# Optimization experiments

Hardware: AMD Instinct MI355X
Metric: run time of the kernel (lower is better)

Reference implementation:

```python
import jax, jax.numpy as jnp
import numpy as np

SIGMA = 0.2
BN_EPS = 1e-5


def setup_inputs() -> dict:
    key = jax.random.key(0)
    k1, k2, k3, k4 = jax.random.split(key, 4)
    B, F, K, M = 8, 16384, 3, 64
    normals = jax.random.normal(k1, (B, 3, F), dtype=jnp.float32)
    # normalize to unit vectors (face normals), keeps math well-conditioned
    normals = normals / jnp.linalg.norm(normals, axis=1, keepdims=True)
    weight_alpha = jax.random.uniform(k2, (1, M, 4), dtype=jnp.float32) * np.pi
    weight_beta = jax.random.uniform(k3, (1, M, 4), dtype=jnp.float32) * 2 * np.pi
    bn_gamma = jnp.ones((M,), dtype=jnp.float32)
    bn_beta = jnp.zeros((M,), dtype=jnp.float32)
    neighbor_index = jax.random.randint(k4, (B, F, K), 0, F, dtype=jnp.int64)
    return {"normals": normals, "weight_alpha": weight_alpha,
            "weight_beta": weight_beta, "bn_gamma": bn_gamma,
            "bn_beta": bn_beta, "neighbor_index": neighbor_index}


def reference(normals, weight_alpha, weight_beta, bn_gamma, bn_beta, neighbor_index):
    # normals: [B, 3, F]; neighbor_index: [B, F, K]
    B, _, F = normals.shape
    K = neighbor_index.shape[-1]
    # kernel points on unit sphere from spherical angles: [3, M, 4]
    sa, ca = jnp.sin(weight_alpha), jnp.cos(weight_alpha)
    sb, cb = jnp.sin(weight_beta), jnp.cos(weight_beta)
    w = jnp.concatenate([sa * cb, sa * sb, ca], axis=0)  # [3, M, 4]

    nt = jnp.transpose(normals, (0, 2, 1))  # [B, F, 3]
    # gather neighbor normals per batch: [B, F, K, 3]
    neigh = jax.vmap(lambda n, idx: n[idx])(nt, neighbor_index)
    # points per face: center + K neighbors -> [B, F, K+1, 3]
    pts = jnp.concatenate([nt[:, :, None, :], neigh], axis=2)

    # squared distance via expansion: ||p||^2 + ||w||^2 - 2 p.w
    dot = jnp.einsum('bfic,cmj->bmfij', pts, w)        # [B, M, F, K+1, 4]
    p2 = jnp.sum(pts * pts, axis=-1)                   # [B, F, K+1]
    w2 = jnp.sum(w * w, axis=0)                        # [M, 4]
    dist = (p2[:, None, :, :, None] + w2[None, :, None, None, :] - 2.0 * dot)

    feat = jnp.sum(jnp.exp(dist / (-2.0 * SIGMA ** 2)), axis=(3, 4))
    feat = feat / float((K + 1) * 4)                   # [B, M, F]

    # BatchNorm1d (training-mode batch stats over B and F per channel M)
    mean = jnp.mean(feat, axis=(0, 2), keepdims=True)
    var = jnp.var(feat, axis=(0, 2), keepdims=True)
    xhat = (feat - mean) / jnp.sqrt(var + BN_EPS)
    out = xhat * bn_gamma[None, :, None] + bn_beta[None, :, None]
    return jax.nn.relu(out)
```

## Files before the change

kernel.cpp:

```cpp
#include <hip/hip_runtime.h>

#define B_DIM 8
#define F_DIM 16384
#define K_DIM 3
#define M_DIM 64
#define MCH   16
#define LOG2E 1.4426950408889634f

#define WS_Q 16384

__global__ __launch_bounds__(256, 4) void fkc_feat_kernel(
    const float* __restrict__ normals,
    const float* __restrict__ walpha,
    const float* __restrict__ wbeta,
    const int*   __restrict__ nidx,
    float* __restrict__ feat_out,
    float* __restrict__ ws)
{
    __shared__ float4 sW[MCH * 4];
    __shared__ float sRS[MCH][32];
    __shared__ float sRQ[MCH][32];

    const int tid = threadIdx.x;
    const int b  = blockIdx.x >> 7;
    const int mc = (blockIdx.x >> 5) & 3;
    const int fc = blockIdx.x & 31;

    if (tid < MCH * 4) {
        int idx = mc * MCH * 4 + tid;
        float a = walpha[idx], bb = wbeta[idx];
        float sa = sinf(a), ca = cosf(a);
        float sb = sinf(bb), cb = cosf(bb);
        float wx = sa * cb, wy = sa * sb, wz = ca;
        float w2 = wx * wx + wy * wy + wz * wz;
        sW[tid] = make_float4(wx * 25.0f * LOG2E, wy * 25.0f * LOG2E,
                              wz * 25.0f * LOG2E, -12.5f * LOG2E * (w2 + 1.0f));
    }
    __syncthreads();

    const int f0 = (fc << 9) + tid * 2;
    const float* nb = normals + (size_t)b * 3 * F_DIM;

    float pxA[4], pyA[4], pzA[4], pxB[4], pyB[4], pzB[4];
    {
        float2 vx = *(const float2*)(nb + f0);
        float2 vy = *(const float2*)(nb + F_DIM + f0);
        float2 vz = *(const float2*)(nb + 2 * F_DIM + f0);
        pxA[0] = vx.x; pxB[0] = vx.y;
        pyA[0] = vy.x; pyB[0] = vy.y;
        pzA[0] = vz.x; pzB[0] = vz.y;
    }
    {
        const int* ib = nidx + ((size_t)b * F_DIM + f0) * K_DIM;
#pragma unroll
        for (int k = 0; k < K_DIM; ++k) {
            int id = ib[k];
            pxA[k + 1] = nb[id]; pyA[k + 1] = nb[F_DIM + id]; pzA[k + 1] = nb[2 * F_DIM + id];
            id = ib[k + 3];
            pxB[k + 1] = nb[id]; pyB[k + 1] = nb[F_DIM + id]; pzB[k + 1] = nb[2 * F_DIM + id];
        }
    }

    const int wave = tid >> 6, lane = tid & 63;
    float* outb = feat_out + ((size_t)b * M_DIM + mc * MCH) * F_DIM + f0;
#pragma unroll 2
    for (int m = 0; m < MCH; ++m) {
        float a0 = 0.f, a1 = 0.f, a2 = 0.f, a3 = 0.f;
        float b0 = 0.f, b1 = 0.f, b2 = 0.f, b3 = 0.f;
#pragma unroll
        for (int j = 0; j < 4; ++j) {
            float4 w = sW[m * 4 + j];
            a0 += __builtin_amdgcn_exp2f(fmaf(w.x, pxA[0], fmaf(w.y, pyA[0], fmaf(w.z, pzA[0], w.w))));
            a1 += __builtin_amdgcn_exp2f(fmaf(w.x, pxA[1], fmaf(w.y, pyA[1], fmaf(w.z, pzA[1], w.w))));
            a2 += __builtin_amdgcn_exp2f(fmaf(w.x, pxA[2], fmaf(w.y, pyA[2], fmaf(w.z, pzA[2], w.w))));
            a3 += __builtin_amdgcn_exp2f(fmaf(w.x, pxA[3], fmaf(w.y, pyA[3], fmaf(w.z, pzA[3], w.w))));
            b0 += __builtin_amdgcn_exp2f(fmaf(w.x, pxB[0], fmaf(w.y, pyB[0], fmaf(w.z, pzB[0], w.w))));
            b1 += __builtin_amdgcn_exp2f(fmaf(w.x, pxB[1], fmaf(w.y, pyB[1], fmaf(w.z, pzB[1], w.w))));
            b2 += __builtin_amdgcn_exp2f(fmaf(w.x, pxB[2], fmaf(w.y, pyB[2], fmaf(w.z, pzB[2], w.w))));
            b3 += __builtin_amdgcn_exp2f(fmaf(w.x, pxB[3], fmaf(w.y, pyB[3], fmaf(w.z, pzB[3], w.w))));
        }
        float fA = ((a0 + a1) + (a2 + a3)) * (1.0f / 16.0f);
        float fB = ((b0 + b1) + (b2 + b3)) * (1.0f / 16.0f);
        *(float2*)(outb + (size_t)m * F_DIM) = make_float2(fA, fB);

        float s = fA + fB;
        float q = fA * fA + fB * fB;
        s += __shfl_xor(s, 8, 64);  q += __shfl_xor(q, 8, 64);
        s += __shfl_xor(s, 16, 64); q += __shfl_xor(q, 16, 64);
        s += __shfl_xor(s, 32, 64); q += __shfl_xor(q, 32, 64);
        if (lane < 8) { sRS[m][wave * 8 + lane] = s; sRQ[m][wave * 8 + lane] = q; }
    }
    __syncthreads();

    {
        const int m = tid >> 4, j = tid & 15;
        float s = sRS[m][j] + sRS[m][j + 16];
        float q = sRQ[m][j] + sRQ[m][j + 16];
        s += __shfl_xor(s, 1, 64);  q += __shfl_xor(q, 1, 64);
        s += __shfl_xor(s, 2, 64);  q += __shfl_xor(q, 2, 64);
        s += __shfl_xor(s, 4, 64);  q += __shfl_xor(q, 4, 64);
        s += __shfl_xor(s, 8, 64);  q += __shfl_xor(q, 8, 64);
        if (j == 0) {
            int slot = (mc * MCH + m) * 256 + b * 32 + fc;
            ws[slot] = s;
            ws[WS_Q + slot] = q;
        }
    }
}

__global__ __launch_bounds__(256) void fkc_bn_kernel(
    float* __restrict__ out,
    const float* __restrict__ gamma,
    const float* __restrict__ beta,
    const float* __restrict__ ws)
{
    __shared__ float sS[4], sQ[4];
    __shared__ float sAC[2];
    const int row = blockIdx.x;
    const int m = row & 63;
    const int tid = threadIdx.x;
    const int wave = tid >> 6, lane = tid & 63;

    {
        float s = ws[m * 256 + tid];
        float q = ws[WS_Q + m * 256 + tid];
#pragma unroll
        for (int off = 32; off >= 1; off >>= 1) {
            s += __shfl_xor(s, off, 64);
            q += __shfl_xor(q, off, 64);
        }
        if (lane == 0) { sS[wave] = s; sQ[wave] = q; }
    }
    __syncthreads();
    if (tid == 0) {
        float s = (sS[0] + sS[1]) + (sS[2] + sS[3]);
        float q = (sQ[0] + sQ[1]) + (sQ[2] + sQ[3]);
        const float invcnt = 1.0f / (float)(B_DIM * F_DIM);
        float mean = s * invcnt;
        float var  = q * invcnt - mean * mean;
        float inv  = rsqrtf(var + 1e-5f);
        float A = gamma[m] * inv;
        sAC[0] = A;
        sAC[1] = beta[m] - mean * A;
    }
    __syncthreads();

    const float A = sAC[0], C = sAC[1];
    float4* p4 = (float4*)(out + (size_t)row * F_DIM);
#pragma unroll
    for (int i = 0; i < 16; ++i) {
        float4 v = p4[tid + i * 256];
        v.x = fmaxf(fmaf(v.x, A, C), 0.0f);
        v.y = fmaxf(fmaf(v.y, A, C), 0.0f);
        v.z = fmaxf(fmaf(v.z, A, C), 0.0f);
        v.w = fmaxf(fmaf(v.w, A, C), 0.0f);
        p4[tid + i * 256] = v;
    }
}

extern "C" void kernel_launch(void* const* d_in, const int* in_sizes, int n_in,
                              void* d_out, int out_size, void* d_ws, size_t ws_size,
                              hipStream_t stream)
{
    const float* normals = (const float*)d_in[0];
    const float* walpha  = (const float*)d_in[1];
    const float* wbeta   = (const float*)d_in[2];
    const float* gamma   = (const float*)d_in[3];
    const float* beta    = (const float*)d_in[4];
    const int*   nidx    = (const int*)d_in[5];
    float* out = (float*)d_out;
    float* ws  = (float*)d_ws;

    hipLaunchKernelGGL(fkc_feat_kernel, dim3(1024), dim3(256), 0, stream,
                       normals, walpha, wbeta, nidx, out, ws);
    hipLaunchKernelGGL(fkc_bn_kernel, dim3(B_DIM * M_DIM), dim3(256), 0, stream,
                       out, gamma, beta, ws);
}
```

Before: 53.19 us.

## Precompute kernel-point table in separate launch and halve channel chunk per block

Weight trig is moved into a tiny one-block kernel that writes a float4 table to the workspace. The feature kernel reads it through global/scalar loads instead of an LDS staging step with a block barrier. The channel chunk drops from 16 to 8, doubling the grid to 2048 blocks with higher occupancy bounds, and the m loop is fully unrolled. The 1/16 scaling is folded into the BN kernel's affine constants. The cost is an extra kernel launch and a second read of the neighbor gathers per block, since each face's gathers are now repeated across 8 channel chunks instead of 4.

```diff
diff --git a/kernel.cpp b/kernel.cpp
--- a/kernel.cpp
+++ b/kernel.cpp
@@ -4,39 +4,41 @@
 #define F_DIM 16384
 #define K_DIM 3
 #define M_DIM 64
-#define MCH   16
+#define MCH   8
 #define LOG2E 1.4426950408889634f
 
 #define WS_Q 16384
+#define WS_W 32768
 
-__global__ __launch_bounds__(256, 4) void fkc_feat_kernel(
-    const float* __restrict__ normals,
-    const float* __restrict__ walpha,
-    const float* __restrict__ wbeta,
-    const int*   __restrict__ nidx,
+__global__ void fkc_wtab_kernel(const float* __restrict__ walpha,
+                                const float* __restrict__ wbeta,
+                                float* __restrict__ ws)
+{
+    const int t = threadIdx.x;
+    float a = walpha[t], b = wbeta[t];
+    float sa = sinf(a), ca = cosf(a);
+    float sb = sinf(b), cb = cosf(b);
+    float wx = sa * cb, wy = sa * sb, wz = ca;
+    float w2 = wx * wx + wy * wy + wz * wz;
+    ((float4*)(ws + WS_W))[t] =
+        make_float4(wx * 25.0f * LOG2E, wy * 25.0f * LOG2E,
+                    wz * 25.0f * LOG2E, -12.5f * LOG2E * (w2 + 1.0f));
+}
+
+__global__ __launch_bounds__(256, 8) void fkc_feat_kernel(
+    const float*  __restrict__ normals,
+    const int*    __restrict__ nidx,
+    const float4* __restrict__ wtab,
     float* __restrict__ feat_out,
     float* __restrict__ ws)
 {
-    __shared__ float4 sW[MCH * 4];
     __shared__ float sRS[MCH][32];
     __shared__ float sRQ[MCH][32];
 
     const int tid = threadIdx.x;
-    const int b  = blockIdx.x >> 7;
-    const int mc = (blockIdx.x >> 5) & 3;
+    const int b  = blockIdx.x >> 8;
+    const int mc = (blockIdx.x >> 5) & 7;
     const int fc = blockIdx.x & 31;
-
-    if (tid < MCH * 4) {
-        int idx = mc * MCH * 4 + tid;
-        float a = walpha[idx], bb = wbeta[idx];
-        float sa = sinf(a), ca = cosf(a);
-        float sb = sinf(bb), cb = cosf(bb);
-        float wx = sa * cb, wy = sa * sb, wz = ca;
-        float w2 = wx * wx + wy * wy + wz * wz;
-        sW[tid] = make_float4(wx * 25.0f * LOG2E, wy * 25.0f * LOG2E,
-                              wz * 25.0f * LOG2E, -12.5f * LOG2E * (w2 + 1.0f));
-    }
-    __syncthreads();
 
     const int f0 = (fc << 9) + tid * 2;
     const float* nb = normals + (size_t)b * 3 * F_DIM;
@@ -62,14 +64,16 @@
     }
 
     const int wave = tid >> 6, lane = tid & 63;
+    const float4* wt = wtab + mc * (MCH * 4);
     float* outb = feat_out + ((size_t)b * M_DIM + mc * MCH) * F_DIM + f0;
-#pragma unroll 2
+
+#pragma unroll
     for (int m = 0; m < MCH; ++m) {
         float a0 = 0.f, a1 = 0.f, a2 = 0.f, a3 = 0.f;
         float b0 = 0.f, b1 = 0.f, b2 = 0.f, b3 = 0.f;
 #pragma unroll
         for (int j = 0; j < 4; ++j) {
-            float4 w = sW[m * 4 + j];
+            float4 w = wt[m * 4 + j];
             a0 += __builtin_amdgcn_exp2f(fmaf(w.x, pxA[0], fmaf(w.y, pyA[0], fmaf(w.z, pzA[0], w.w))));
             a1 += __builtin_amdgcn_exp2f(fmaf(w.x, pxA[1], fmaf(w.y, pyA[1], fmaf(w.z, pzA[1], w.w))));
             a2 += __builtin_amdgcn_exp2f(fmaf(w.x, pxA[2], fmaf(w.y, pyA[2], fmaf(w.z, pzA[2], w.w))));
@@ -79,12 +83,12 @@
             b2 += __builtin_amdgcn_exp2f(fmaf(w.x, pxB[2], fmaf(w.y, pyB[2], fmaf(w.z, pzB[2], w.w))));
             b3 += __builtin_amdgcn_exp2f(fmaf(w.x, pxB[3], fmaf(w.y, pyB[3], fmaf(w.z, pzB[3], w.w))));
         }
-        float fA = ((a0 + a1) + (a2 + a3)) * (1.0f / 16.0f);
-        float fB = ((b0 + b1) + (b2 + b3)) * (1.0f / 16.0f);
-        *(float2*)(outb + (size_t)m * F_DIM) = make_float2(fA, fB);
+        float SA = (a0 + a1) + (a2 + a3);
+        float SB = (b0 + b1) + (b2 + b3);
+        *(float2*)(outb + (size_t)m * F_DIM) = make_float2(SA, SB);
 
-        float s = fA + fB;
-        float q = fA * fA + fB * fB;
+        float s = SA + SB;
+        float q = SA * SA + SB * SB;
         s += __shfl_xor(s, 8, 64);  q += __shfl_xor(q, 8, 64);
         s += __shfl_xor(s, 16, 64); q += __shfl_xor(q, 16, 64);
         s += __shfl_xor(s, 32, 64); q += __shfl_xor(q, 32, 64);
@@ -92,7 +96,7 @@
     }
     __syncthreads();
 
-    {
+    if (tid < MCH * 16) {
         const int m = tid >> 4, j = tid & 15;
         float s = sRS[m][j] + sRS[m][j + 16];
         float q = sRQ[m][j] + sRQ[m][j + 16];
@@ -136,12 +140,14 @@
         float s = (sS[0] + sS[1]) + (sS[2] + sS[3]);
         float q = (sQ[0] + sQ[1]) + (sQ[2] + sQ[3]);
         const float invcnt = 1.0f / (float)(B_DIM * F_DIM);
-        float mean = s * invcnt;
-        float var  = q * invcnt - mean * mean;
-        float inv  = rsqrtf(var + 1e-5f);
+        float meanS = s * invcnt;
+        float meanF = meanS * (1.0f / 16.0f);
+        float ef2   = q * invcnt * (1.0f / 256.0f);
+        float var   = ef2 - meanF * meanF;
+        float inv   = rsqrtf(var + 1e-5f);
         float A = gamma[m] * inv;
-        sAC[0] = A;
-        sAC[1] = beta[m] - mean * A;
+        sAC[0] = A * (1.0f / 16.0f);
+        sAC[1] = beta[m] - meanF * A;
     }
     __syncthreads();
 
@@ -171,8 +177,10 @@
     float* out = (float*)d_out;
     float* ws  = (float*)d_ws;
 
-    hipLaunchKernelGGL(fkc_feat_kernel, dim3(1024), dim3(256), 0, stream,
-                       normals, walpha, wbeta, nidx, out, ws);
+    hipLaunchKernelGGL(fkc_wtab_kernel, dim3(1), dim3(256), 0, stream,
+                       walpha, wbeta, ws);
+    hipLaunchKernelGGL(fkc_feat_kernel, dim3(2048), dim3(256), 0, stream,
+                       normals, nidx, (const float4*)(ws + WS_W), out, ws);
     hipLaunchKernelGGL(fkc_bn_kernel, dim3(B_DIM * M_DIM), dim3(256), 0, stream,
                        out, gamma, beta, ws);
 }
```

After: 60.95 us. 1.15x slower.
